# Performance work log

Measured on AMD Instinct MI355X. Metric: run time of the kernel, lower is better.

The kernel has to match this reference:

```python
import jax, jax.numpy as jnp
import numpy as np

L, D, H, T, B = 4, 512, 8, 1024, 8
FF = 4 * D          # 2048
E = 2
EC = E * D          # 1024 conv channels
K = 31
W = 64              # attention window
DH = D // H
EPS = 1e-5


def _ln(x, g, b):
    m = jnp.mean(x, axis=-1, keepdims=True)
    v = jnp.mean((x - m) ** 2, axis=-1, keepdims=True)
    return (x - m) * jax.lax.rsqrt(v + EPS) * g + b


def setup_inputs() -> dict:
    key = jax.random.key(0)
    ks = iter(jax.random.split(key, 64))
    n = lambda shape, s=0.02: jax.random.normal(next(ks), shape, dtype=jnp.float32) * s
    inp = {
        'x': jax.random.normal(next(ks), (B, T, D), dtype=jnp.float32),
        # FFN1 (half residual)
        'ffn1_ln_g': jnp.ones((L, D)), 'ffn1_ln_b': jnp.zeros((L, D)),
        'ffn1_w1': n((L, D, FF)), 'ffn1_b1': jnp.zeros((L, FF)),
        'ffn1_w2': n((L, FF, D)), 'ffn1_b2': jnp.zeros((L, D)),
        # local MHSA
        'attn_ln_g': jnp.ones((L, D)), 'attn_ln_b': jnp.zeros((L, D)),
        'qkv_w': n((L, D, 3 * D)), 'qkv_b': jnp.zeros((L, 3 * D)),
        'outp_w': n((L, D, D)), 'outp_b': jnp.zeros((L, D)),
        # conv module
        'conv_ln_g': jnp.ones((L, D)), 'conv_ln_b': jnp.zeros((L, D)),
        'pw1_w': n((L, D, 2 * EC)), 'pw1_b': jnp.zeros((L, 2 * EC)),
        'dw_w': n((L, EC, 1, K), 0.1), 'dw_b': jnp.zeros((L, EC)),
        'gn_g': jnp.ones((L, EC)), 'gn_b': jnp.zeros((L, EC)),
        'pw2_w': n((L, EC, D)), 'pw2_b': jnp.zeros((L, D)),
        # FFN2 (half residual)
        'ffn2_ln_g': jnp.ones((L, D)), 'ffn2_ln_b': jnp.zeros((L, D)),
        'ffn2_w1': n((L, D, FF)), 'ffn2_b1': jnp.zeros((L, FF)),
        'ffn2_w2': n((L, FF, D)), 'ffn2_b2': jnp.zeros((L, D)),
        # per-block final LN and decoder final LN
        'blk_ln_g': jnp.ones((L, D)), 'blk_ln_b': jnp.zeros((L, D)),
        'final_ln_g': jnp.ones((D,)), 'final_ln_b': jnp.zeros((D,)),
    }
    return inp


def _forward(x, ffn1_ln_g, ffn1_ln_b, ffn1_w1, ffn1_b1, ffn1_w2, ffn1_b2,
             attn_ln_g, attn_ln_b, qkv_w, qkv_b, outp_w, outp_b,
             conv_ln_g, conv_ln_b, pw1_w, pw1_b, dw_w, dw_b, gn_g, gn_b, pw2_w, pw2_b,
             ffn2_ln_g, ffn2_ln_b, ffn2_w1, ffn2_b1, ffn2_w2, ffn2_b2,
             blk_ln_g, blk_ln_b, final_ln_g, final_ln_b):
    t = jnp.arange(T)
    local_ok = jnp.abs(t[:, None] - t[None, :]) <= (W // 2)   # [T,T] banded window mask
    scale = DH ** -0.5

    for l in range(L):
        # ---- FFN1 (half residual), SiLU ----
        h = _ln(x, ffn1_ln_g[l], ffn1_ln_b[l])
        h = jax.nn.silu(h @ ffn1_w1[l] + ffn1_b1[l]) @ ffn1_w2[l] + ffn1_b2[l]
        x = x + 0.5 * h

        # ---- local windowed MHSA ----
        a = _ln(x, attn_ln_g[l], attn_ln_b[l])
        qkv = (a @ qkv_w[l] + qkv_b[l]).reshape(B, T, 3, H, DH)
        q, k, v = (qkv[:, :, 0].transpose(0, 2, 1, 3),  # [B,H,T,DH]
                   qkv[:, :, 1].transpose(0, 2, 1, 3),
                   qkv[:, :, 2].transpose(0, 2, 1, 3))
        scores = jnp.einsum('bhqd,bhkd->bhqk', q, k) * scale
        scores = jnp.where(local_ok, scores, -jnp.inf)
        attn = jax.nn.softmax(scores, axis=-1)
        o = jnp.einsum('bhqk,bhkd->bhqd', attn, v)
        o = o.transpose(0, 2, 1, 3).reshape(B, T, D)
        x = x + (o @ outp_w[l] + outp_b[l])

        # ---- convolution module ----
        c = _ln(x, conv_ln_g[l], conv_ln_b[l])
        c = c @ pw1_w[l] + pw1_b[l]                 # [B,T,2EC]
        c = c[..., :EC] * jax.nn.sigmoid(c[..., EC:])  # GLU (channel halves)
        c = c.transpose(0, 2, 1)                    # [B,EC,T]
        c = jax.lax.conv_general_dilated(
            c, dw_w[l], window_strides=(1,), padding=[((K - 1) // 2, (K - 1) // 2)],
            dimension_numbers=('NCH', 'OIH', 'NCH'), feature_group_count=EC)
        c = c + dw_b[l][None, :, None]
        # GroupNorm(num_groups=1): normalize over (C,T) per sample
        m = jnp.mean(c, axis=(1, 2), keepdims=True)
        vv = jnp.mean((c - m) ** 2, axis=(1, 2), keepdims=True)
        c = (c - m) * jax.lax.rsqrt(vv + EPS) * gn_g[l][None, :, None] + gn_b[l][None, :, None]
        c = jax.nn.silu(c)
        c = c.transpose(0, 2, 1) @ pw2_w[l] + pw2_b[l]  # [B,T,D]
        x = x + c

        # ---- FFN2 (half residual) ----
        h = _ln(x, ffn2_ln_g[l], ffn2_ln_b[l])
        h = jax.nn.silu(h @ ffn2_w1[l] + ffn2_b1[l]) @ ffn2_w2[l] + ffn2_b2[l]
        x = x + 0.5 * h

        # ---- per-block final LayerNorm ----
        x = _ln(x, blk_ln_g[l], blk_ln_b[l])

    return _ln(x, final_ln_g, final_ln_b)


def reference(x, ffn1_ln_g, ffn1_ln_b, ffn1_w1, ffn1_b1, ffn1_w2, ffn1_b2,
              attn_ln_g, attn_ln_b, qkv_w, qkv_b, outp_w, outp_b,
              conv_ln_g, conv_ln_b, pw1_w, pw1_b, dw_w, dw_b, gn_g, gn_b, pw2_w, pw2_b,
              ffn2_ln_g, ffn2_ln_b, ffn2_w1, ffn2_b1, ffn2_w2, ffn2_b2,
              blk_ln_g, blk_ln_b, final_ln_g, final_ln_b):
    return _forward(x, ffn1_ln_g, ffn1_ln_b, ffn1_w1, ffn1_b1, ffn1_w2, ffn1_b2,
                    attn_ln_g, attn_ln_b, qkv_w, qkv_b, outp_w, outp_b,
                    conv_ln_g, conv_ln_b, pw1_w, pw1_b, dw_w, dw_b, gn_g, gn_b, pw2_w, pw2_b,
                    ffn2_ln_g, ffn2_ln_b, ffn2_w1, ffn2_b1, ffn2_w2, ffn2_b2,
                    blk_ln_g, blk_ln_b, final_ln_g, final_ln_b)
```

## Files before the change

### kernel.cpp

```cpp
#include <hip/hip_runtime.h>
#include <hip/hip_bf16.h>
#include <math.h>

#define L_ 4
#define D_ 512
#define H_ 8
#define T_ 1024
#define B_ 8
#define FF_ 2048
#define EC_ 1024
#define KW_ 31
#define DH_ 64
#define ROWS (B_*T_)

typedef __attribute__((ext_vector_type(8))) short short8;
typedef __attribute__((ext_vector_type(4))) float f32x4;
typedef __attribute__((ext_vector_type(4))) unsigned short ushort4v;
typedef __attribute__((ext_vector_type(2))) unsigned short ushort2v;

static __device__ __forceinline__ unsigned short f2bf(float f) {
  __hip_bfloat16 h = __float2bfloat16(f);
  unsigned short u;
  __builtin_memcpy(&u, &h, 2);
  return u;
}
static __device__ __forceinline__ float bf2f(unsigned short h) {
  union { unsigned u; float f; } v; v.u = ((unsigned)h) << 16;
  return v.f;
}
static __device__ __forceinline__ float sigm(float x) {
  return __builtin_amdgcn_rcpf(1.0f + __expf(-x));
}

#define GLDS(gp, lp) __builtin_amdgcn_global_load_lds( \
    (const __attribute__((address_space(1))) unsigned int*)(const void*)(gp), \
    (__attribute__((address_space(3))) unsigned int*)(void*)(lp), 16, 0, 0)

#define SW8(row, slot) ((slot) ^ (((row) ^ ((row) >> 3)) & 7))

__global__ __launch_bounds__(256) void cvt_ln_kernel(const float* __restrict__ in,
    const float* __restrict__ g, const float* __restrict__ b,
    unsigned short* __restrict__ x, unsigned short* __restrict__ y)
{
  int row = blockIdx.x * 4 + (threadIdx.x >> 6);
  int l = threadIdx.x & 63;
  const float* ir = in + (size_t)row * D_ + l * 8;
  float4 v0 = *(const float4*)ir;
  float4 v1 = *(const float4*)(ir + 4);
  float raw[8] = {v0.x, v0.y, v0.z, v0.w, v1.x, v1.y, v1.z, v1.w};
  short8 xo;
  float vv[8];
#pragma unroll
  for (int j = 0; j < 8; ++j) {
    unsigned short h = f2bf(raw[j]);
    xo[j] = (short)h;
    vv[j] = bf2f(h);
  }
  *(short8*)(x + (size_t)row * D_ + l * 8) = xo;
  float s = 0.f, s2 = 0.f;
#pragma unroll
  for (int j = 0; j < 8; ++j) { s += vv[j]; s2 += vv[j] * vv[j]; }
#pragma unroll
  for (int off = 32; off; off >>= 1) {
    s  += __shfl_xor(s,  off, 64);
    s2 += __shfl_xor(s2, off, 64);
  }
  float mean = s * (1.0f / D_);
  float var  = s2 * (1.0f / D_) - mean * mean;
  float r = __builtin_amdgcn_rsqf(var + 1e-5f);
  float4 g0 = *(const float4*)(g + l * 8);
  float4 g1 = *(const float4*)(g + l * 8 + 4);
  float4 b0 = *(const float4*)(b + l * 8);
  float4 b1 = *(const float4*)(b + l * 8 + 4);
  float gg[8] = {g0.x, g0.y, g0.z, g0.w, g1.x, g1.y, g1.z, g1.w};
  float bb[8] = {b0.x, b0.y, b0.z, b0.w, b1.x, b1.y, b1.z, b1.w};
  short8 o;
#pragma unroll
  for (int j = 0; j < 8; ++j) o[j] = (short)f2bf((vv[j] - mean) * r * gg[j] + bb[j]);
  *(short8*)(y + (size_t)row * D_ + l * 8) = o;
}

__global__ __launch_bounds__(256) void ln_bf16_kernel(const unsigned short* __restrict__ x,
    const float* __restrict__ g, const float* __restrict__ b, unsigned short* __restrict__ y)
{
  int row = blockIdx.x * 4 + (threadIdx.x >> 6);
  int l = threadIdx.x & 63;
  short8 xr = *(const short8*)(x + (size_t)row * D_ + l * 8);
  float vv[8];
#pragma unroll
  for (int j = 0; j < 8; ++j) vv[j] = bf2f((unsigned short)xr[j]);
  float s = 0.f, s2 = 0.f;
#pragma unroll
  for (int j = 0; j < 8; ++j) { s += vv[j]; s2 += vv[j] * vv[j]; }
#pragma unroll
  for (int off = 32; off; off >>= 1) {
    s  += __shfl_xor(s,  off, 64);
    s2 += __shfl_xor(s2, off, 64);
  }
  float mean = s * (1.0f / D_);
  float var  = s2 * (1.0f / D_) - mean * mean;
  float r = __builtin_amdgcn_rsqf(var + 1e-5f);
  float4 g0 = *(const float4*)(g + l * 8);
  float4 g1 = *(const float4*)(g + l * 8 + 4);
  float4 b0 = *(const float4*)(b + l * 8);
  float4 b1 = *(const float4*)(b + l * 8 + 4);
  float gg[8] = {g0.x, g0.y, g0.z, g0.w, g1.x, g1.y, g1.z, g1.w};
  float bb[8] = {b0.x, b0.y, b0.z, b0.w, b1.x, b1.y, b1.z, b1.w};
  short8 o;
#pragma unroll
  for (int j = 0; j < 8; ++j) o[j] = (short)f2bf((vv[j] - mean) * r * gg[j] + bb[j]);
  *(short8*)(y + (size_t)row * D_ + l * 8) = o;
}

template<bool BF2>
__global__ __launch_bounds__(256) void ln_dual_kernel(const unsigned short* __restrict__ x,
    const float* __restrict__ g1, const float* __restrict__ b1,
    const float* __restrict__ g2, const float* __restrict__ b2,
    unsigned short* __restrict__ y1, void* __restrict__ y2)
{
  int row = blockIdx.x * 4 + (threadIdx.x >> 6);
  int l = threadIdx.x & 63;
  short8 xr = *(const short8*)(x + (size_t)row * D_ + l * 8);
  float vv[8];
#pragma unroll
  for (int j = 0; j < 8; ++j) vv[j] = bf2f((unsigned short)xr[j]);
  float s = 0.f, s2 = 0.f;
#pragma unroll
  for (int j = 0; j < 8; ++j) { s += vv[j]; s2 += vv[j] * vv[j]; }
#pragma unroll
  for (int off = 32; off; off >>= 1) {
    s  += __shfl_xor(s,  off, 64);
    s2 += __shfl_xor(s2, off, 64);
  }
  float mean = s * (1.0f / D_);
  float var  = s2 * (1.0f / D_) - mean * mean;
  float r = __builtin_amdgcn_rsqf(var + 1e-5f);
  float4 g0 = *(const float4*)(g1 + l * 8);
  float4 g1v = *(const float4*)(g1 + l * 8 + 4);
  float4 b0 = *(const float4*)(b1 + l * 8);
  float4 b1v = *(const float4*)(b1 + l * 8 + 4);
  float ga[8] = {g0.x, g0.y, g0.z, g0.w, g1v.x, g1v.y, g1v.z, g1v.w};
  float ba[8] = {b0.x, b0.y, b0.z, b0.w, b1v.x, b1v.y, b1v.z, b1v.w};
  float yv[8];
  float u = 0.f, u2 = 0.f;
#pragma unroll
  for (int j = 0; j < 8; ++j) {
    yv[j] = (vv[j] - mean) * r * ga[j] + ba[j];
    u += yv[j]; u2 += yv[j] * yv[j];
  }
  {
    short8 o;
#pragma unroll
    for (int j = 0; j < 8; ++j) o[j] = (short)f2bf(yv[j]);
    *(short8*)(y1 + (size_t)row * D_ + l * 8) = o;
  }
#pragma unroll
  for (int off = 32; off; off >>= 1) {
    u  += __shfl_xor(u,  off, 64);
    u2 += __shfl_xor(u2, off, 64);
  }
  float mean2 = u * (1.0f / D_);
  float var2  = u2 * (1.0f / D_) - mean2 * mean2;
  float r2 = __builtin_amdgcn_rsqf(var2 + 1e-5f);
  float4 c0 = *(const float4*)(g2 + l * 8);
  float4 c1 = *(const float4*)(g2 + l * 8 + 4);
  float4 d0 = *(const float4*)(b2 + l * 8);
  float4 d1 = *(const float4*)(b2 + l * 8 + 4);
  float gc[8] = {c0.x, c0.y, c0.z, c0.w, c1.x, c1.y, c1.z, c1.w};
  float bc[8] = {d0.x, d0.y, d0.z, d0.w, d1.x, d1.y, d1.z, d1.w};
  if constexpr (BF2) {
    short8 o;
#pragma unroll
    for (int j = 0; j < 8; ++j) o[j] = (short)f2bf((yv[j] - mean2) * r2 * gc[j] + bc[j]);
    *(short8*)((unsigned short*)y2 + (size_t)row * D_ + l * 8) = o;
  } else {
    float z[8];
#pragma unroll
    for (int j = 0; j < 8; ++j) z[j] = (yv[j] - mean2) * r2 * gc[j] + bc[j];
    float4 o0 = {z[0], z[1], z[2], z[3]};
    float4 o1 = {z[4], z[5], z[6], z[7]};
    float* yp = (float*)y2 + (size_t)row * D_ + l * 8;
    *(float4*)yp = o0; *(float4*)(yp + 4) = o1;
  }
}

__global__ __launch_bounds__(256) void wtr_kernel(const float* __restrict__ W,
    unsigned short* __restrict__ Wt, int K, int N)
{
  __shared__ float tile[32][33];
  const float* Wl = W + (size_t)blockIdx.z * K * N;
  unsigned short* Wtl = Wt + (size_t)blockIdx.z * K * N;
  int n0 = blockIdx.x * 32, k0 = blockIdx.y * 32;
  int c = threadIdx.x & 31, r = threadIdx.x >> 5;
#pragma unroll
  for (int it = 0; it < 4; ++it) {
    int kk = r + it * 8;
    tile[kk][c] = Wl[(size_t)(k0 + kk) * N + n0 + c];
  }
  __syncthreads();
#pragma unroll
  for (int it = 0; it < 4; ++it) {
    int nn = r + it * 8;
    Wtl[(size_t)(n0 + nn) * K + k0 + c] = f2bf(tile[c][nn]);
  }
}

template<int EPI>
__global__ __launch_bounds__(256) void gemm_mfma(
    const unsigned short* __restrict__ A, const unsigned short* __restrict__ Wt,
    const float* __restrict__ bias, void* __restrict__ Cv,
    int N, int K)
{
  constexpr int TM = 128;
  constexpr int AI = TM / 32;
  __shared__ __align__(16) unsigned short As[3][TM * 32];
  __shared__ __align__(16) unsigned short Bs[3][128 * 32];
  int t = threadIdx.x;
  int gx = gridDim.x;
  int nwg = gx * gridDim.y;
  int orig = blockIdx.y * gx + blockIdx.x;
  int lg = (orig & 7) * (nwg >> 3) + (orig >> 3);
  int row0 = (lg / gx) * TM;
  int col0 = (lg % gx) * (EPI == 3 ? 64 : 128);
  int l = t & 63, w = t >> 6, wm = w >> 1, wn = w & 1;

  int ar0 = t >> 2;
  int sa0 = (t & 3) ^ ((ar0 >> 1) & 3);
  int ar1 = (t + 256) >> 2;
  int sa1 = (t & 3) ^ ((ar1 >> 1) & 3);
  const unsigned short* agp0 = A + (size_t)(row0 + ar0) * K + sa0 * 8;
  const unsigned short* agp1 = A + (size_t)(row0 + ar1) * K + sa1 * 8;
  const unsigned short* bgp0 = Wt + (size_t)(col0 + ar0) * K + sa0 * 8;
  const unsigned short* bgp1 =
      (EPI == 3) ? Wt + (size_t)(EC_ + col0 + (ar1 - 64)) * K + sa1 * 8
                 : Wt + (size_t)(col0 + ar1) * K + sa1 * 8;

  int lrow = (l >> 4) * 4, lcol = l & 15, kq = l >> 4;
  int aoff[AI], boff[4];
#pragma unroll
  for (int i = 0; i < AI; ++i) {
    int row = wm * (TM / 2) + i * 16 + lcol;
    aoff[i] = (row * 4 + (kq ^ ((row >> 1) & 3))) * 8;
  }
#pragma unroll
  for (int j = 0; j < 4; ++j) {
    int row;
    if constexpr (EPI == 3)
      row = (j < 2 ? wn * 32 + j * 16 : 64 + wn * 32 + (j - 2) * 16) + lcol;
    else
      row = wn * 64 + j * 16 + lcol;
    boff[j] = (row * 4 + (kq ^ ((row >> 1) & 3))) * 8;
  }

  f32x4 acc[AI][4] = {};
  int nt = K >> 5;

  auto stage = [&](int buf) {
    GLDS(agp0, As[buf] + t * 8);
    GLDS(agp1, As[buf] + (t + 256) * 8);
    GLDS(bgp0, Bs[buf] + t * 8);
    GLDS(bgp1, Bs[buf] + (t + 256) * 8);
    agp0 += 32; agp1 += 32; bgp0 += 32; bgp1 += 32;
  };
  stage(0); stage(1);
  int cur = 0, nxt = 2;

  for (int kt = 0; kt < nt; ++kt) {
    if (kt < nt - 1) asm volatile("s_waitcnt vmcnt(4)" ::: "memory");
    else             asm volatile("s_waitcnt vmcnt(0)" ::: "memory");
    __builtin_amdgcn_s_barrier();
    __builtin_amdgcn_sched_barrier(0);
    if (kt + 2 < nt) { stage(nxt); nxt = (nxt == 2) ? 0 : nxt + 1; }
    const unsigned short* Ab = As[cur];
    const unsigned short* Bb = Bs[cur];
    cur = (cur == 2) ? 0 : cur + 1;
    short8 af[AI], bfr[4];
#pragma unroll
    for (int i = 0; i < AI; ++i) af[i]  = *(const short8*)(Ab + aoff[i]);
#pragma unroll
    for (int j = 0; j < 4; ++j) bfr[j] = *(const short8*)(Bb + boff[j]);
    __builtin_amdgcn_s_setprio(1);
#pragma unroll
    for (int i = 0; i < AI; ++i)
#pragma unroll
      for (int j = 0; j < 4; ++j)
        acc[i][j] = __builtin_amdgcn_mfma_f32_16x16x32_bf16(af[i], bfr[j], acc[i][j], 0, 0, 0);
    __builtin_amdgcn_s_setprio(0);
  }

  if constexpr (EPI == 3) {
    float bja[2], bjg[2];
#pragma unroll
    for (int j = 0; j < 2; ++j) {
      int c = col0 + wn * 32 + j * 16 + lcol;
      bja[j] = bias[c];
      bjg[j] = bias[EC_ + c];
    }
#pragma unroll
    for (int i = 0; i < AI; ++i) {
      int gr0 = row0 + wm * (TM / 2) + i * 16 + lrow;
#pragma unroll
      for (int j = 0; j < 2; ++j) {
        int gc = col0 + wn * 32 + j * 16 + lcol;
#pragma unroll
        for (int q = 0; q < 4; ++q) {
          float a = acc[i][j][q] + bja[j];
          float g = acc[i][j + 2][q] + bjg[j];
          ((unsigned short*)Cv)[(size_t)(gr0 + q) * N + gc] = f2bf(a * sigm(g));
        }
      }
    }
  } else {
    float bj[4];
#pragma unroll
    for (int j = 0; j < 4; ++j) bj[j] = bias[col0 + wn * 64 + j * 16 + lcol];
#pragma unroll
    for (int i = 0; i < AI; ++i) {
      int gr0 = row0 + wm * (TM / 2) + i * 16 + lrow;
#pragma unroll
      for (int j = 0; j < 4; ++j) {
        int gc = col0 + wn * 64 + j * 16 + lcol;
#pragma unroll
        for (int q = 0; q < 4; ++q) {
          float v = acc[i][j][q] + bj[j];
          size_t off = (size_t)(gr0 + q) * N + gc;
          if constexpr (EPI == 0) {
            ((unsigned short*)Cv)[off] = f2bf(v);
          } else {
            ((unsigned short*)Cv)[off] = f2bf(v * sigm(v));
          }
        }
      }
    }
  }
}

__global__ __launch_bounds__(256) void gemm_res64(
    const unsigned short* __restrict__ A, const unsigned short* __restrict__ Wt,
    const float* __restrict__ bias, const unsigned short* __restrict__ R,
    unsigned short* __restrict__ C, int N, int K, float alpha)
{
  __shared__ __align__(16) unsigned short As[3][64 * 64];
  __shared__ __align__(16) unsigned short Bs[3][128 * 64];
  int t = threadIdx.x;
  int gx = gridDim.x;
  int nwg = gx * gridDim.y;
  int orig = blockIdx.y * gx + blockIdx.x;
  int lg = (orig & 7) * (nwg >> 3) + (orig >> 3);
  int row0 = (lg / gx) * 64;
  int col0 = (lg % gx) * 128;
  int l = t & 63, w = t >> 6, wm = w >> 1, wn = w & 1;

  int arA0 = t >> 3;
  int sA0  = (t & 7) ^ (arA0 & 7);
  int cA1  = t + 256;
  int arA1 = cA1 >> 3;
  int sA1  = (cA1 & 7) ^ (arA1 & 7);
  const unsigned short* agp0 = A + (size_t)(row0 + arA0) * K + sA0 * 8;
  const unsigned short* agp1 = A + (size_t)(row0 + arA1) * K + sA1 * 8;
  const unsigned short* bgp[4];
#pragma unroll
  for (int q = 0; q < 4; ++q) {
    int c = t + q * 256;
    int r = c >> 3, s = (c & 7) ^ (r & 7);
    bgp[q] = Wt + (size_t)(col0 + r) * K + s * 8;
  }

  int lcol = l & 15, kq = l >> 4, lrow = kq * 4;
  int aoff[2][2], boff[4][2];
#pragma unroll
  for (int i = 0; i < 2; ++i) {
    int row = wm * 32 + i * 16 + lcol;
#pragma unroll
    for (int kk = 0; kk < 2; ++kk)
      aoff[i][kk] = row * 64 + (((kk * 4 + kq) ^ (row & 7)) * 8);
  }
#pragma unroll
  for (int j = 0; j < 4; ++j) {
    int row = wn * 64 + j * 16 + lcol;
#pragma unroll
    for (int kk = 0; kk < 2; ++kk)
      boff[j][kk] = row * 64 + (((kk * 4 + kq) ^ (row & 7)) * 8);
  }

  f32x4 acc[2][4] = {};
  int nt = K >> 6;

  auto stage = [&](int buf) {
    GLDS(agp0, As[buf] + t * 8);
    GLDS(agp1, As[buf] + (t + 256) * 8);
#pragma unroll
    for (int q = 0; q < 4; ++q) GLDS(bgp[q], Bs[buf] + (t + q * 256) * 8);
    agp0 += 64; agp1 += 64;
#pragma unroll
    for (int q = 0; q < 4; ++q) bgp[q] += 64;
  };
  stage(0); stage(1);
  int cur = 0, nxt = 2;

  for (int kt = 0; kt < nt; ++kt) {
    if (kt < nt - 1) asm volatile("s_waitcnt vmcnt(6)" ::: "memory");
    else             asm volatile("s_waitcnt vmcnt(0)" ::: "memory");
    __builtin_amdgcn_s_barrier();
    __builtin_amdgcn_sched_barrier(0);
    if (kt + 2 < nt) { stage(nxt); nxt = (nxt == 2) ? 0 : nxt + 1; }
    const unsigned short* Ab = As[cur];
    const unsigned short* Bb = Bs[cur];
    cur = (cur == 2) ? 0 : cur + 1;
    short8 af[2][2], bfr[4][2];
#pragma unroll
    for (int i = 0; i < 2; ++i)
#pragma unroll
      for (int kk = 0; kk < 2; ++kk) af[i][kk] = *(const short8*)(Ab + aoff[i][kk]);
#pragma unroll
    for (int j = 0; j < 4; ++j)
#pragma unroll
      for (int kk = 0; kk < 2; ++kk) bfr[j][kk] = *(const short8*)(Bb + boff[j][kk]);
    __builtin_amdgcn_s_setprio(1);
#pragma unroll
    for (int kk = 0; kk < 2; ++kk)
#pragma unroll
      for (int i = 0; i < 2; ++i)
#pragma unroll
        for (int j = 0; j < 4; ++j)
          acc[i][j] = __builtin_amdgcn_mfma_f32_16x16x32_bf16(af[i][kk], bfr[j][kk],
                                                              acc[i][j], 0, 0, 0);
    __builtin_amdgcn_s_setprio(0);
  }

  float bj[4];
#pragma unroll
  for (int j = 0; j < 4; ++j) bj[j] = bias[col0 + wn * 64 + j * 16 + lcol];
#pragma unroll
  for (int i = 0; i < 2; ++i) {
    int gr0 = row0 + wm * 32 + i * 16 + lrow;
#pragma unroll
    for (int j = 0; j < 4; ++j) {
      int gc = col0 + wn * 64 + j * 16 + lcol;
#pragma unroll
      for (int q = 0; q < 4; ++q) {
        size_t off = (size_t)(gr0 + q) * N + gc;
        C[off] = f2bf(bf2f(R[off]) + alpha * (acc[i][j][q] + bj[j]));
      }
    }
  }
}

__global__ __launch_bounds__(256) void attn_kernel(const unsigned short* __restrict__ QKV,
                                                   unsigned short* __restrict__ O)
{
  __shared__ __align__(16) unsigned short Ks[128 * 64];
  __shared__ __align__(16) unsigned short Vt[64 * 128];
  __shared__ __align__(16) unsigned short Ps[64 * 128];
  int qt = blockIdx.x, h = blockIdx.y, b = blockIdx.z;
  int t = threadIdx.x;
  int l = t & 63, w = t >> 6;
  int q0 = qt * 64;
  int jbase = q0 - 32;

#pragma unroll
  for (int i = 0; i < 4; ++i) {
    int c = t + i * 256;
    int row = c >> 3, sl = c & 7;
    int jg = jbase + row;
    short8 kv = {};
    if ((unsigned)jg < (unsigned)T_)
      kv = *(const short8*)(QKV + ((size_t)(b * T_ + jg)) * 1536 + 512 + h * DH_ + sl * 8);
    *(short8*)(Ks + row * 64 + SW8(row, sl) * 8) = kv;
  }
#pragma unroll
  for (int i = 0; i < 4; ++i) {
    int c = t + i * 256;
    int row = c >> 3, d0 = (c & 7) * 8;
    int jg = jbase + row;
    short8 vv = {};
    if ((unsigned)jg < (unsigned)T_)
      vv = *(const short8*)(QKV + ((size_t)(b * T_ + jg)) * 1536 + 1024 + h * DH_ + d0);
#pragma unroll
    for (int q = 0; q < 8; ++q) {
      int d = d0 + q;
      Vt[d * 128 + SW8(d, row >> 3) * 8 + (row & 7)] = (unsigned short)vv[q];
    }
  }
  short8 qf[2];
#pragma unroll
  for (int ks = 0; ks < 2; ++ks)
    qf[ks] = *(const short8*)(QKV + ((size_t)(b * T_ + q0 + w * 16 + (l & 15))) * 1536
                              + h * DH_ + ks * 32 + (l >> 4) * 8);
  __syncthreads();

  f32x4 sacc[8] = {};
  __builtin_amdgcn_s_setprio(1);
#pragma unroll
  for (int jt = 0; jt < 8; ++jt) {
#pragma unroll
    for (int ks = 0; ks < 2; ++ks) {
      int row = jt * 16 + (l & 15);
      int sl = ks * 4 + (l >> 4);
      short8 kf = *(const short8*)(Ks + row * 64 + SW8(row, sl) * 8);
      sacc[jt] = __builtin_amdgcn_mfma_f32_16x16x32_bf16(qf[ks], kf, sacc[jt], 0, 0, 0);
    }
  }
  __builtin_amdgcn_s_setprio(0);

  const float scale = 0.125f;
  int qgl0 = q0 + w * 16 + ((l >> 4) << 2);
  int jl = jbase + (l & 15);
  float m4[4] = {-3.0e38f, -3.0e38f, -3.0e38f, -3.0e38f};
#pragma unroll
  for (int jt = 0; jt < 8; ++jt) {
#pragma unroll
    for (int r = 0; r < 4; ++r) {
      float s = sacc[jt][r] * scale;
      int jg = jl + jt * 16;
      int dd = jg - (qgl0 + r);
      bool ok = ((unsigned)jg < (unsigned)T_) && (dd <= 32) && (dd >= -32);
      s = ok ? s : -3.0e38f;
      sacc[jt][r] = s;
      m4[r] = fmaxf(m4[r], s);
    }
  }
#pragma unroll
  for (int r = 0; r < 4; ++r) {
    m4[r] = fmaxf(m4[r], __shfl_xor(m4[r], 1, 64));
    m4[r] = fmaxf(m4[r], __shfl_xor(m4[r], 2, 64));
    m4[r] = fmaxf(m4[r], __shfl_xor(m4[r], 4, 64));
    m4[r] = fmaxf(m4[r], __shfl_xor(m4[r], 8, 64));
  }
  float sum4[4] = {0.f, 0.f, 0.f, 0.f};
#pragma unroll
  for (int jt = 0; jt < 8; ++jt) {
#pragma unroll
    for (int r = 0; r < 4; ++r) {
      float e = __expf(sacc[jt][r] - m4[r]);
      sum4[r] += e;
      int qrow = w * 16 + ((l >> 4) << 2) + r;
      int j = jt * 16 + (l & 15);
      Ps[qrow * 128 + SW8(qrow, j >> 3) * 8 + (j & 7)] = f2bf(e);
    }
  }
#pragma unroll
  for (int r = 0; r < 4; ++r) {
    sum4[r] += __shfl_xor(sum4[r], 1, 64);
    sum4[r] += __shfl_xor(sum4[r], 2, 64);
    sum4[r] += __shfl_xor(sum4[r], 4, 64);
    sum4[r] += __shfl_xor(sum4[r], 8, 64);
    sum4[r] = __builtin_amdgcn_rcpf(sum4[r]);
  }

  f32x4 oacc[4] = {};
  __builtin_amdgcn_s_setprio(1);
#pragma unroll
  for (int ks = 0; ks < 4; ++ks) {
    int prow = w * 16 + (l & 15);
    int sl = ks * 4 + (l >> 4);
    short8 pf = *(const short8*)(Ps + prow * 128 + SW8(prow, sl) * 8);
#pragma unroll
    for (int dt = 0; dt < 4; ++dt) {
      int vrow = dt * 16 + (l & 15);
      short8 vf = *(const short8*)(Vt + vrow * 128 + SW8(vrow, sl) * 8);
      oacc[dt] = __builtin_amdgcn_mfma_f32_16x16x32_bf16(pf, vf, oacc[dt], 0, 0, 0);
    }
  }
  __builtin_amdgcn_s_setprio(0);
#pragma unroll
  for (int dt = 0; dt < 4; ++dt) {
#pragma unroll
    for (int r = 0; r < 4; ++r) {
      int qg = q0 + w * 16 + ((l >> 4) << 2) + r;
      int d = dt * 16 + (l & 15);
      O[((size_t)(b * T_ + qg)) * D_ + h * DH_ + d] = f2bf(oacc[dt][r] * sum4[r]);
    }
  }
}

#define TT_ 16
__global__ __launch_bounds__(256) void dwconv_kernel(const unsigned short* __restrict__ X,
    const float* __restrict__ w, const float* __restrict__ bias,
    unsigned short* __restrict__ Y, float* __restrict__ red)
{
  int t = threadIdx.x;
  int gid = blockIdx.x;
  int ecb = gid & 1;
  int tt  = (gid >> 1) & 63;
  int b   = gid >> 7;
  int e0 = ecb * 512 + t * 2;
  int t0 = tt * TT_;
  const unsigned short* xp = X + (size_t)b * T_ * EC_ + e0;

  float wr0[KW_], wr1[KW_];
#pragma unroll
  for (int k = 0; k < KW_; ++k) { wr0[k] = w[e0 * KW_ + k]; wr1[k] = w[(e0 + 1) * KW_ + k]; }
  float out0[TT_], out1[TT_];
  float bv0 = bias[e0], bv1 = bias[e0 + 1];
#pragma unroll
  for (int i = 0; i < TT_; ++i) { out0[i] = bv0; out1[i] = bv1; }

#pragma unroll
  for (int j = 0; j < TT_ + KW_ - 1; ++j) {
    int tj = t0 - 15 + j;
    float x0 = 0.f, x1 = 0.f;
    if ((unsigned)tj < (unsigned)T_) {
      ushort2v u = *(const ushort2v*)(xp + (size_t)tj * EC_);
      x0 = bf2f(u.x); x1 = bf2f(u.y);
    }
#pragma unroll
    for (int i = 0; i < TT_; ++i) {
      int k = j - i;
      if (k >= 0 && k < KW_) {
        out0[i] = fmaf(x0, wr0[k], out0[i]);
        out1[i] = fmaf(x1, wr1[k], out1[i]);
      }
    }
  }
  unsigned short* yp = Y + ((size_t)b * T_ + t0) * EC_ + e0;
  float s = 0.f, s2 = 0.f;
#pragma unroll
  for (int i = 0; i < TT_; ++i) {
    ushort2v o; o.x = f2bf(out0[i]); o.y = f2bf(out1[i]);
    *(ushort2v*)(yp + (size_t)i * EC_) = o;
    s += out0[i] + out1[i];
    s2 += out0[i] * out0[i] + out1[i] * out1[i];
  }
#pragma unroll
  for (int off = 32; off; off >>= 1) {
    s  += __shfl_down(s,  off, 64);
    s2 += __shfl_down(s2, off, 64);
  }
  __shared__ float rs[4], rq[4];
  if ((t & 63) == 0) { rs[t >> 6] = s; rq[t >> 6] = s2; }
  __syncthreads();
  if (t == 0) {
    int loc = gid & 127;
    red[(b * 128 + loc) * 2]     = rs[0] + rs[1] + rs[2] + rs[3];
    red[(b * 128 + loc) * 2 + 1] = rq[0] + rq[1] + rq[2] + rq[3];
  }
}

__global__ __launch_bounds__(256) void gn_stats_kernel(const float* __restrict__ partial,
                                                       float* __restrict__ stats)
{
  int b = blockIdx.x, t = threadIdx.x;
  float s = 0.f, s2 = 0.f;
  if (t < 128) {
    s  = partial[b * 256 + t * 2];
    s2 = partial[b * 256 + t * 2 + 1];
  }
#pragma unroll
  for (int off = 32; off; off >>= 1) {
    s  += __shfl_down(s,  off, 64);
    s2 += __shfl_down(s2, off, 64);
  }
  __shared__ float rs[4], rq[4];
  if ((t & 63) == 0) { rs[t >> 6] = s; rq[t >> 6] = s2; }
  __syncthreads();
  if (t == 0) {
    float S = rs[0] + rs[1] + rs[2] + rs[3];
    float S2 = rq[0] + rq[1] + rq[2] + rq[3];
    const float n = (float)(T_ * EC_);
    float mean = S / n;
    float var  = S2 / n - mean * mean;
    stats[b * 2]     = mean;
    stats[b * 2 + 1] = __builtin_amdgcn_rsqf(var + 1e-5f);
  }
}

__global__ __launch_bounds__(256) void gn_apply_kernel(const unsigned short* __restrict__ X,
    const float* __restrict__ stats, const float* __restrict__ g, const float* __restrict__ bb,
    unsigned short* __restrict__ out)
{
  int idx = blockIdx.x * 256 + threadIdx.x;
  int e8 = (idx & 127) << 3;
  int bt = idx >> 7;
  int b  = bt >> 10;
  float mean = stats[b * 2], rstd = stats[b * 2 + 1];
  short8 v = *(const short8*)(X + (size_t)idx * 8);
  float4 g0 = *(const float4*)(g + e8);
  float4 g1 = *(const float4*)(g + e8 + 4);
  float4 b0 = *(const float4*)(bb + e8);
  float4 b1 = *(const float4*)(bb + e8 + 4);
  float gg[8] = {g0.x, g0.y, g0.z, g0.w, g1.x, g1.y, g1.z, g1.w};
  float bv[8] = {b0.x, b0.y, b0.z, b0.w, b1.x, b1.y, b1.z, b1.w};
  short8 o;
#pragma unroll
  for (int j = 0; j < 8; ++j) {
    float u = (bf2f((unsigned short)v[j]) - mean) * rstd * gg[j] + bv[j];
    o[j] = (short)f2bf(u * sigm(u));
  }
  *(short8*)(out + (size_t)idx * 8) = o;
}

extern "C" void kernel_launch(void* const* d_in, const int* in_sizes, int n_in,
                              void* d_out, int out_size, void* d_ws, size_t ws_size,
                              hipStream_t stream)
{
  const float* in_x      = (const float*)d_in[0];
  const float* ffn1_ln_g = (const float*)d_in[1];
  const float* ffn1_ln_b = (const float*)d_in[2];
  const float* ffn1_w1   = (const float*)d_in[3];
  const float* ffn1_b1   = (const float*)d_in[4];
  const float* ffn1_w2   = (const float*)d_in[5];
  const float* ffn1_b2   = (const float*)d_in[6];
  const float* attn_ln_g = (const float*)d_in[7];
  const float* attn_ln_b = (const float*)d_in[8];
  const float* qkv_w     = (const float*)d_in[9];
  const float* qkv_b     = (const float*)d_in[10];
  const float* outp_w    = (const float*)d_in[11];
  const float* outp_b    = (const float*)d_in[12];
  const float* conv_ln_g = (const float*)d_in[13];
  const float* conv_ln_b = (const float*)d_in[14];
  const float* pw1_w     = (const float*)d_in[15];
  const float* pw1_b     = (const float*)d_in[16];
  const float* dw_w      = (const float*)d_in[17];
  const float* dw_b      = (const float*)d_in[18];
  const float* gn_g      = (const float*)d_in[19];
  const float* gn_b      = (const float*)d_in[20];
  const float* pw2_w     = (const float*)d_in[21];
  const float* pw2_b     = (const float*)d_in[22];
  const float* ffn2_ln_g = (const float*)d_in[23];
  const float* ffn2_ln_b = (const float*)d_in[24];
  const float* ffn2_w1   = (const float*)d_in[25];
  const float* ffn2_b1   = (const float*)d_in[26];
  const float* ffn2_w2   = (const float*)d_in[27];
  const float* ffn2_b2   = (const float*)d_in[28];
  const float* blk_ln_g  = (const float*)d_in[29];
  const float* blk_ln_b  = (const float*)d_in[30];
  const float* fin_ln_g  = (const float*)d_in[31];
  const float* fin_ln_b  = (const float*)d_in[32];

  char* p = (char*)d_ws;
  unsigned short* x    = (unsigned short*)p; p += (size_t)ROWS * D_ * 2;
  unsigned short* big3 = (unsigned short*)p; p += (size_t)ROWS * EC_ * 2;
  float* red  = (float*)p;          p += 8192 * 4;
  unsigned short* abuf  = (unsigned short*)p; p += (size_t)ROWS * D_ * 2;
  unsigned short* inner = (unsigned short*)p; p += (size_t)ROWS * FF_ * 2;
  unsigned short* big2  = (unsigned short*)p; p += (size_t)ROWS * EC_ * 2;
  unsigned short* wt_w1a = (unsigned short*)p; p += (size_t)L_ * D_ * FF_ * 2;
  unsigned short* wt_w1b = (unsigned short*)p; p += (size_t)L_ * FF_ * D_ * 2;
  unsigned short* wt_qkv = (unsigned short*)p; p += (size_t)L_ * D_ * 1536 * 2;
  unsigned short* wt_out = (unsigned short*)p; p += (size_t)L_ * D_ * D_ * 2;
  unsigned short* wt_pw1 = (unsigned short*)p; p += (size_t)L_ * D_ * 2048 * 2;
  unsigned short* wt_pw2 = (unsigned short*)p; p += (size_t)L_ * EC_ * D_ * 2;
  unsigned short* wt_w2a = (unsigned short*)p; p += (size_t)L_ * D_ * FF_ * 2;
  unsigned short* wt_w2b = (unsigned short*)p; p += (size_t)L_ * FF_ * D_ * 2;
  float* stats = red + 4096;

  dim3 blk256(256);
  cvt_ln_kernel<<<ROWS/4, blk256, 0, stream>>>(in_x, ffn1_ln_g, ffn1_ln_b, x, abuf);

  wtr_kernel<<<dim3(FF_/32,  D_/32,  L_), blk256, 0, stream>>>(ffn1_w1, wt_w1a, D_, FF_);
  wtr_kernel<<<dim3(D_/32,   FF_/32, L_), blk256, 0, stream>>>(ffn1_w2, wt_w1b, FF_, D_);
  wtr_kernel<<<dim3(1536/32, D_/32,  L_), blk256, 0, stream>>>(qkv_w,   wt_qkv, D_, 1536);
  wtr_kernel<<<dim3(D_/32,   D_/32,  L_), blk256, 0, stream>>>(outp_w,  wt_out, D_, D_);
  wtr_kernel<<<dim3(2048/32, D_/32,  L_), blk256, 0, stream>>>(pw1_w,   wt_pw1, D_, 2048);
  wtr_kernel<<<dim3(D_/32,   EC_/32, L_), blk256, 0, stream>>>(pw2_w,   wt_pw2, EC_, D_);
  wtr_kernel<<<dim3(FF_/32,  D_/32,  L_), blk256, 0, stream>>>(ffn2_w1, wt_w2a, D_, FF_);
  wtr_kernel<<<dim3(D_/32,   FF_/32, L_), blk256, 0, stream>>>(ffn2_w2, wt_w2b, FF_, D_);

  for (int l = 0; l < L_; ++l) {
    gemm_mfma<1><<<dim3(FF_/128, ROWS/128), blk256, 0, stream>>>(
        abuf, wt_w1a + (size_t)l*D_*FF_, ffn1_b1 + l*FF_, inner, FF_, D_);
    gemm_res64<<<dim3(D_/128, ROWS/64), blk256, 0, stream>>>(
        inner, wt_w1b + (size_t)l*FF_*D_, ffn1_b2 + l*D_, x, x, D_, FF_, 0.5f);

    ln_bf16_kernel<<<ROWS/4, blk256, 0, stream>>>(x, attn_ln_g + l*D_, attn_ln_b + l*D_, abuf);
    gemm_mfma<0><<<dim3(1536/128, ROWS/128), blk256, 0, stream>>>(
        abuf, wt_qkv + (size_t)l*D_*1536, qkv_b + l*1536, inner, 1536, D_);
    attn_kernel<<<dim3(T_/64, H_, B_), blk256, 0, stream>>>(inner, abuf);
    gemm_res64<<<dim3(D_/128, ROWS/64), blk256, 0, stream>>>(
        abuf, wt_out + (size_t)l*D_*D_, outp_b + l*D_, x, x, D_, D_, 1.0f);

    ln_bf16_kernel<<<ROWS/4, blk256, 0, stream>>>(x, conv_ln_g + l*D_, conv_ln_b + l*D_, abuf);
    gemm_mfma<3><<<dim3(EC_/64, ROWS/128), blk256, 0, stream>>>(
        abuf, wt_pw1 + (size_t)l*D_*2048, pw1_b + l*2048, big2, EC_, D_);
    dwconv_kernel<<<B_ * (T_/TT_) * (EC_/512), blk256, 0, stream>>>(
        big2, dw_w + (size_t)l*EC_*KW_, dw_b + l*EC_, big3, red);
    gn_stats_kernel<<<B_, blk256, 0, stream>>>(red, stats);
    gn_apply_kernel<<<(ROWS * EC_ / 8) / 256, blk256, 0, stream>>>(
        big3, stats, gn_g + l*EC_, gn_b + l*EC_, big2);
    gemm_res64<<<dim3(D_/128, ROWS/64), blk256, 0, stream>>>(
        big2, wt_pw2 + (size_t)l*EC_*D_, pw2_b + l*D_, x, x, D_, EC_, 1.0f);

    ln_bf16_kernel<<<ROWS/4, blk256, 0, stream>>>(x, ffn2_ln_g + l*D_, ffn2_ln_b + l*D_, abuf);
    gemm_mfma<1><<<dim3(FF_/128, ROWS/128), blk256, 0, stream>>>(
        abuf, wt_w2a + (size_t)l*D_*FF_, ffn2_b1 + l*FF_, inner, FF_, D_);
    gemm_res64<<<dim3(D_/128, ROWS/64), blk256, 0, stream>>>(
        inner, wt_w2b + (size_t)l*FF_*D_, ffn2_b2 + l*D_, x, x, D_, FF_, 0.5f);

    if (l < L_ - 1) {
      ln_dual_kernel<true><<<ROWS/4, blk256, 0, stream>>>(
          x, blk_ln_g + l*D_, blk_ln_b + l*D_,
          ffn1_ln_g + (l+1)*D_, ffn1_ln_b + (l+1)*D_, x, abuf);
    } else {
      ln_dual_kernel<false><<<ROWS/4, blk256, 0, stream>>>(
          x, blk_ln_g + l*D_, blk_ln_b + l*D_, fin_ln_g, fin_ln_b, x, d_out);
    }
  }
}
```

Measured before the change: 1.156 ms.

## Deepen GEMM K-tile to 64 with double buffering and 8-way swizzle

```diff
diff --git a/kernel.cpp b/kernel.cpp
--- a/kernel.cpp
+++ b/kernel.cpp
@@ -211,36 +211,41 @@
     const float* __restrict__ bias, void* __restrict__ Cv,
     int N, int K)
 {
-  constexpr int TM = 128;
-  constexpr int AI = TM / 32;
-  __shared__ __align__(16) unsigned short As[3][TM * 32];
-  __shared__ __align__(16) unsigned short Bs[3][128 * 32];
+  constexpr int AI = 4;
+  __shared__ __align__(16) unsigned short As[2][128 * 64];
+  __shared__ __align__(16) unsigned short Bs[2][128 * 64];
   int t = threadIdx.x;
   int gx = gridDim.x;
   int nwg = gx * gridDim.y;
   int orig = blockIdx.y * gx + blockIdx.x;
   int lg = (orig & 7) * (nwg >> 3) + (orig >> 3);
-  int row0 = (lg / gx) * TM;
+  int row0 = (lg / gx) * 128;
   int col0 = (lg % gx) * (EPI == 3 ? 64 : 128);
   int l = t & 63, w = t >> 6, wm = w >> 1, wn = w & 1;
 
-  int ar0 = t >> 2;
-  int sa0 = (t & 3) ^ ((ar0 >> 1) & 3);
-  int ar1 = (t + 256) >> 2;
-  int sa1 = (t & 3) ^ ((ar1 >> 1) & 3);
-  const unsigned short* agp0 = A + (size_t)(row0 + ar0) * K + sa0 * 8;
-  const unsigned short* agp1 = A + (size_t)(row0 + ar1) * K + sa1 * 8;
-  const unsigned short* bgp0 = Wt + (size_t)(col0 + ar0) * K + sa0 * 8;
-  const unsigned short* bgp1 =
-      (EPI == 3) ? Wt + (size_t)(EC_ + col0 + (ar1 - 64)) * K + sa1 * 8
-                 : Wt + (size_t)(col0 + ar1) * K + sa1 * 8;
-
-  int lrow = (l >> 4) * 4, lcol = l & 15, kq = l >> 4;
-  int aoff[AI], boff[4];
+  const unsigned short* agp[4];
+  const unsigned short* bgp[4];
+#pragma unroll
+  for (int q = 0; q < 4; ++q) {
+    int c = t + q * 256;
+    int row = c >> 3, s = (c & 7) ^ (row & 7);
+    agp[q] = A + (size_t)(row0 + row) * K + s * 8;
+    int brow;
+    if constexpr (EPI == 3)
+      brow = (row < 64) ? (col0 + row) : (EC_ + col0 + (row - 64));
+    else
+      brow = col0 + row;
+    bgp[q] = Wt + (size_t)brow * K + s * 8;
+  }
+
+  int lcol = l & 15, kq = l >> 4, lrow = kq * 4;
+  int aoff[AI][2], boff[4][2];
 #pragma unroll
   for (int i = 0; i < AI; ++i) {
-    int row = wm * (TM / 2) + i * 16 + lcol;
-    aoff[i] = (row * 4 + (kq ^ ((row >> 1) & 3))) * 8;
+    int row = wm * 64 + i * 16 + lcol;
+#pragma unroll
+    for (int kk = 0; kk < 2; ++kk)
+      aoff[i][kk] = row * 64 + (((kk * 4 + kq) ^ (row & 7)) * 8);
   }
 #pragma unroll
   for (int j = 0; j < 4; ++j) {
@@ -249,43 +254,54 @@
       row = (j < 2 ? wn * 32 + j * 16 : 64 + wn * 32 + (j - 2) * 16) + lcol;
     else
       row = wn * 64 + j * 16 + lcol;
-    boff[j] = (row * 4 + (kq ^ ((row >> 1) & 3))) * 8;
+#pragma unroll
+    for (int kk = 0; kk < 2; ++kk)
+      boff[j][kk] = row * 64 + (((kk * 4 + kq) ^ (row & 7)) * 8);
   }
 
   f32x4 acc[AI][4] = {};
-  int nt = K >> 5;
+  int nt = K >> 6;
 
   auto stage = [&](int buf) {
-    GLDS(agp0, As[buf] + t * 8);
-    GLDS(agp1, As[buf] + (t + 256) * 8);
-    GLDS(bgp0, Bs[buf] + t * 8);
-    GLDS(bgp1, Bs[buf] + (t + 256) * 8);
-    agp0 += 32; agp1 += 32; bgp0 += 32; bgp1 += 32;
+#pragma unroll
+    for (int q = 0; q < 4; ++q) {
+      GLDS(agp[q], As[buf] + (t + q * 256) * 8);
+      GLDS(bgp[q], Bs[buf] + (t + q * 256) * 8);
+      agp[q] += 64; bgp[q] += 64;
+    }
   };
   stage(0); stage(1);
-  int cur = 0, nxt = 2;
 
   for (int kt = 0; kt < nt; ++kt) {
-    if (kt < nt - 1) asm volatile("s_waitcnt vmcnt(4)" ::: "memory");
+    int cur = kt & 1;
+    if (kt < nt - 1) asm volatile("s_waitcnt vmcnt(8)" ::: "memory");
     else             asm volatile("s_waitcnt vmcnt(0)" ::: "memory");
     __builtin_amdgcn_s_barrier();
     __builtin_amdgcn_sched_barrier(0);
-    if (kt + 2 < nt) { stage(nxt); nxt = (nxt == 2) ? 0 : nxt + 1; }
     const unsigned short* Ab = As[cur];
     const unsigned short* Bb = Bs[cur];
-    cur = (cur == 2) ? 0 : cur + 1;
-    short8 af[AI], bfr[4];
-#pragma unroll
-    for (int i = 0; i < AI; ++i) af[i]  = *(const short8*)(Ab + aoff[i]);
-#pragma unroll
-    for (int j = 0; j < 4; ++j) bfr[j] = *(const short8*)(Bb + boff[j]);
+    short8 af[AI][2], bfr[4][2];
+#pragma unroll
+    for (int i = 0; i < AI; ++i)
+#pragma unroll
+      for (int kk = 0; kk < 2; ++kk) af[i][kk] = *(const short8*)(Ab + aoff[i][kk]);
+#pragma unroll
+    for (int j = 0; j < 4; ++j)
+#pragma unroll
+      for (int kk = 0; kk < 2; ++kk) bfr[j][kk] = *(const short8*)(Bb + boff[j][kk]);
     __builtin_amdgcn_s_setprio(1);
 #pragma unroll
-    for (int i = 0; i < AI; ++i)
-#pragma unroll
-      for (int j = 0; j < 4; ++j)
-        acc[i][j] = __builtin_amdgcn_mfma_f32_16x16x32_bf16(af[i], bfr[j], acc[i][j], 0, 0, 0);
+    for (int kk = 0; kk < 2; ++kk)
+#pragma unroll
+      for (int i = 0; i < AI; ++i)
+#pragma unroll
+        for (int j = 0; j < 4; ++j)
+          acc[i][j] = __builtin_amdgcn_mfma_f32_16x16x32_bf16(af[i][kk], bfr[j][kk],
+                                                              acc[i][j], 0, 0, 0);
     __builtin_amdgcn_s_setprio(0);
+    __builtin_amdgcn_s_barrier();
+    __builtin_amdgcn_sched_barrier(0);
+    if (kt + 2 < nt) stage(cur);
   }
 
   if constexpr (EPI == 3) {
@@ -298,7 +314,7 @@
     }
 #pragma unroll
     for (int i = 0; i < AI; ++i) {
-      int gr0 = row0 + wm * (TM / 2) + i * 16 + lrow;
+      int gr0 = row0 + wm * 64 + i * 16 + lrow;
 #pragma unroll
       for (int j = 0; j < 2; ++j) {
         int gc = col0 + wn * 32 + j * 16 + lcol;
@@ -316,7 +332,7 @@
     for (int j = 0; j < 4; ++j) bj[j] = bias[col0 + wn * 64 + j * 16 + lcol];
 #pragma unroll
     for (int i = 0; i < AI; ++i) {
-      int gr0 = row0 + wm * (TM / 2) + i * 16 + lrow;
+      int gr0 = row0 + wm * 64 + i * 16 + lrow;
 #pragma unroll
       for (int j = 0; j < 4; ++j) {
         int gc = col0 + wn * 64 + j * 16 + lcol;
```

Result: faster. 1.114 ms (-3.6%).
